# Kernel optimization log

Measured on AMD Instinct MI355X. Metric: run time of the kernel, lower is better.

Reference implementation:

```python
import jax, jax.numpy as jnp
import numpy as np

EPS = 0.1           # sinkhorn entropic regularizer (epsilon=0.1 in OT())
GAMMA = 1.0         # KL penalty on relaxed (row) marginal (gamma=1)
NUM_SK_ITERS = 3    # num_iters=3, final=False path
RHO_UPPER = 1.0
RHO_BASE = 0.1


def sigmoid_rampup(current, rampup_length):
    if rampup_length == 0:
        return 1.0
    current = np.clip(current, 0.0, rampup_length)
    phase = 1.0 - current / rampup_length
    return float(np.exp(-5.0 * phase * phase))


def set_rho(current, total):
    rho = sigmoid_rampup(current, total) * RHO_UPPER + RHO_BASE
    return min(rho, 1.0)


def setup_inputs() -> dict:
    key = jax.random.key(0)
    kx, ky = jax.random.split(key)
    x = jax.random.normal(kx, (8192, 1024), dtype=jnp.float32)
    y = jax.random.normal(ky, (2048, 1024), dtype=jnp.float32)
    return {"x": x, "y": y, "iterations": 100, "iterations_per_epoch": 20}


def _normalize_feature(x):
    # x = x - x.min(-1)[0].unsqueeze(-1)
    return x - jnp.min(x, axis=-1, keepdims=True)


def _cdist(x, y):
    # torch.cdist with p=2 (Euclidean)
    x2 = jnp.sum(x * x, axis=-1, keepdims=True)          # (N,1)
    y2 = jnp.sum(y * y, axis=-1)                         # (M,)
    d2 = x2 + y2[None, :] - 2.0 * (x @ y.T)              # (N,M)
    return jnp.sqrt(jnp.maximum(d2, 0.0))


def _semi_sinkhorn_stable(cost, rho):
    """Log-domain (stable) semi-relaxed Sinkhorn-Knopp.
    Column marginal is enforced exactly with total mass rho (curriculum mass);
    row marginal is relaxed via KL penalty gamma -> damped f update.
    Returns transport plan with sum(flow) == rho."""
    N, M = cost.shape
    lam = GAMMA / (GAMMA + EPS)
    loga = -np.log(N)                   # uniform row prior (prior=None)
    logb = np.log(rho) - np.log(M)      # uniform column marginal, mass rho
    logK = -cost / EPS                  # (N,M)
    f = jnp.zeros((N,), cost.dtype)
    g = jnp.zeros((M,), cost.dtype)
    lse = jax.scipy.special.logsumexp
    for _ in range(NUM_SK_ITERS):
        f = -lam * EPS * lse(logK + g[None, :] / EPS + logb, axis=1)
        g = -EPS * lse(logK + f[:, None] / EPS + loga, axis=0)
    flow = jnp.exp(logK + f[:, None] / EPS + g[None, :] / EPS + loga + logb)
    return flow


def reference(x, y, iterations, iterations_per_epoch):
    x = _normalize_feature(x)
    y = _normalize_feature(y)
    rho = set_rho(iterations, 10 * iterations_per_epoch)  # sigmoid rho schedule
    cost = _cdist(x, y)
    cost = cost / jnp.max(cost)
    flow = _semi_sinkhorn_stable(cost, rho)
    flow = flow / rho                                      # renormalize to total mass 1
    dist = jnp.sum(cost * flow)
    return flow, dist
```

## Files before the change

### kernel.cpp

```cpp
#include <hip/hip_runtime.h>
#include <math.h>

#define N_ROWS 8192
#define M_COLS 2048
#define K_DIM  1024
#define NM     ((size_t)N_ROWS * M_COLS)

#define LAM       0.9090909090909091f
#define LOG_M     7.624618986159398f

#define SKB 512
#define RPB (N_ROWS / SKB)

typedef __bf16 bf16x8 __attribute__((ext_vector_type(8)));
typedef float  f32x4  __attribute__((ext_vector_type(4)));
typedef unsigned short u16x8 __attribute__((ext_vector_type(8)));
typedef _Float16 h8 __attribute__((ext_vector_type(8)));


static __device__ __forceinline__ size_t xb_off(int i) {
    return ((size_t)(i >> 1) << 13) + 4096 + ((size_t)(i & 1) << 11);
}
static __device__ __forceinline__ size_t yb_off(int j) {
    return ((size_t)1 << 25) + ((size_t)(j >> 1) << 13) + 4096 + ((size_t)(j & 1) << 11);
}

__global__ void k_init(const int* __restrict__ iters, const int* __restrict__ ipe,
                       float* __restrict__ params, float* __restrict__ sigma,
                       unsigned int* __restrict__ d2max, float* __restrict__ dist)
{
    const int t = blockIdx.x * 256 + threadIdx.x;
    if (t < M_COLS) {
        sigma[t] = 0.0f;
        sigma[M_COLS + t] = 0.0f;
        sigma[2 * M_COLS + t] = 0.0f;
    }
    if (t == 0) {
        float ramp = 10.0f * (float)ipe[0];
        float rho;
        if (ramp == 0.0f) {
            rho = 1.1f;
        } else {
            float cur = fminf(fmaxf((float)iters[0], 0.0f), ramp);
            float phase = 1.0f - cur / ramp;
            rho = expf(-5.0f * phase * phase) + 0.1f;
        }
        rho = fminf(rho, 1.0f);
        params[0] = rho;
        params[1] = logf(rho) - LOG_M;
        *d2max = 0u;
        *dist = 0.0f;
    }
}

static __device__ __forceinline__ unsigned pk_bf16(float a, float b) {
#if __has_builtin(__builtin_amdgcn_cvt_pk_bf16_f32)
    typedef __bf16 bf16x2 __attribute__((ext_vector_type(2)));
    bf16x2 r = __builtin_amdgcn_cvt_pk_bf16_f32(a, b);
    return __builtin_bit_cast(unsigned, r);
#else
    unsigned ua = __float_as_uint(a), ub = __float_as_uint(b);
    ua += 0x7FFFu + ((ua >> 16) & 1u);
    ub += 0x7FFFu + ((ub >> 16) & 1u);
    return (ua >> 16) | (ub & 0xFFFF0000u);
#endif
}

static __device__ __forceinline__ bf16x8 lds_frag(const unsigned short* p) {
    return __builtin_bit_cast(bf16x8, *(const u16x8*)p);
}

static __device__ __forceinline__ void gload16(const void* g, void* l) {
    __builtin_amdgcn_global_load_lds(
        (const __attribute__((address_space(1))) unsigned int*)g,
        (__attribute__((address_space(3))) unsigned int*)l, 16, 0, 0);
}

__global__ __launch_bounds__(256) void rowstats_cvt(
    const float* __restrict__ X, const float* __restrict__ Y,
    unsigned char* __restrict__ outb,
    float* __restrict__ mx, float* __restrict__ sx, float* __restrict__ x2,
    float* __restrict__ my, float* __restrict__ sy, float* __restrict__ y2)
{
    const int b = blockIdx.x, tid = threadIdx.x;
    const bool isX = b < N_ROWS;
    const int row = isX ? b : b - N_ROWS;
    const float* src = isX ? (X + (size_t)row * K_DIM) : (Y + (size_t)row * K_DIM);
    const float4 v = ((const float4*)src)[tid];

    uint2 p; p.x = pk_bf16(v.x, v.y); p.y = pk_bf16(v.z, v.w);
    size_t off = isX ? xb_off(row) : yb_off(row);
    *(uint2*)(outb + off + (size_t)tid * 8) = p;

    float lmin = fminf(fminf(v.x, v.y), fminf(v.z, v.w));
    float lsum = v.x + v.y + v.z + v.w;
    float lsq  = v.x*v.x + v.y*v.y + v.z*v.z + v.w*v.w;

    __shared__ float rmin[256], rsum[256], rsq[256];
    rmin[tid] = lmin; rsum[tid] = lsum; rsq[tid] = lsq;
    __syncthreads();
    for (int s = 128; s > 0; s >>= 1) {
        if (tid < s) {
            rmin[tid] = fminf(rmin[tid], rmin[tid + s]);
            rsum[tid] += rsum[tid + s];
            rsq[tid]  += rsq[tid + s];
        }
        __syncthreads();
    }
    if (tid == 0) {
        float m = rmin[0], s = rsum[0], q = rsq[0];
        if (isX) { mx[row] = m; sx[row] = s; x2[row] = q - 2.f*m*s + (float)K_DIM*m*m; }
        else     { my[row] = m; sy[row] = s; y2[row] = q - 2.f*m*s + (float)K_DIM*m*m; }
    }
}

__global__ __launch_bounds__(256, 4) void gemm_cost_mfma(
    float* __restrict__ gbuf,
    const float* __restrict__ mx, const float* __restrict__ sx, const float* __restrict__ x2,
    const float* __restrict__ my, const float* __restrict__ sy, const float* __restrict__ y2,
    unsigned int* __restrict__ d2max)
{
    __shared__ unsigned short Ash[2][128 * 32];
    __shared__ unsigned short Bsh[2][128 * 32];
    __shared__ float rmax[256];

    const unsigned char* outb = (const unsigned char*)gbuf;
    const int tid   = threadIdx.x;
    const int lane  = tid & 63;
    const int wave  = tid >> 6;
    const int wi    = wave >> 1;
    const int wj    = wave & 1;
    const int row16 = lane & 15;
    const int quad  = lane >> 4;

    const int bid0 = blockIdx.y * 16 + blockIdx.x;
    const int bid  = (bid0 & 7) * 128 + (bid0 >> 3);
    const int i0 = (bid >> 4) * 128, j0 = (bid & 15) * 128;

    const int chA = (lane & 3) * 16;
    const unsigned char* pa[2];
    const unsigned char* pb[2];
    unsigned short* laA[2];
    unsigned short* lbB[2];
    #pragma unroll
    for (int p = 0; p < 2; ++p) {
        const int rt = (p * 4 + wave) * 16 + (lane >> 2);
        pa[p] = outb + xb_off(i0 + rt) + chA;
        pb[p] = outb + yb_off(j0 + rt) + chA;
        laA[p] = &Ash[0][(p * 4 + wave) * 512];
        lbB[p] = &Bsh[0][(p * 4 + wave) * 512];
    }

    f32x4 acc[4][4];
    #pragma unroll
    for (int u = 0; u < 4; ++u)
        #pragma unroll
        for (int v = 0; v < 4; ++v) acc[u][v] = (f32x4){0.f, 0.f, 0.f, 0.f};

#define STAGE(nb) do {                                        \
        gload16(pa[0], laA[0] + (nb) * 4096);                 \
        gload16(pa[1], laA[1] + (nb) * 4096);                 \
        gload16(pb[0], lbB[0] + (nb) * 4096);                 \
        gload16(pb[1], lbB[1] + (nb) * 4096);                 \
        pa[0] += 64; pa[1] += 64; pb[0] += 64; pb[1] += 64;   \
    } while (0)

#define COMPUTE(cb) do {                                                         \
        bf16x8 af[4], bfr[4];                                                    \
        _Pragma("unroll")                                                        \
        for (int t = 0; t < 4; ++t) {                                            \
            af[t]  = lds_frag(&Ash[cb][(wi * 64 + t * 16 + row16) * 32 + quad * 8]); \
            bfr[t] = lds_frag(&Bsh[cb][(wj * 64 + t * 16 + row16) * 32 + quad * 8]); \
        }                                                                        \
        _Pragma("unroll")                                                        \
        for (int ti = 0; ti < 4; ++ti)                                           \
            _Pragma("unroll")                                                    \
            for (int tj = 0; tj < 4; ++tj)                                       \
                acc[ti][tj] = __builtin_amdgcn_mfma_f32_16x16x32_bf16(           \
                    af[ti], bfr[tj], acc[ti][tj], 0, 0, 0);                      \
    } while (0)

    STAGE(0);
    __syncthreads();

#pragma unroll 1
    for (int it = 0; it < 15; ++it) {
        STAGE(1); COMPUTE(0); __syncthreads();
        STAGE(0); COMPUTE(1); __syncthreads();
    }
    STAGE(1); COMPUTE(0); __syncthreads();
    COMPUTE(1);

#undef STAGE
#undef COMPUTE

    _Float16* costh = (_Float16*)gbuf;
    float lmax = 0.0f;
    float myj[4], syj[4], yy[4];
    #pragma unroll
    for (int tj = 0; tj < 4; ++tj) {
        const int j = j0 + wj * 64 + tj * 16 + row16;
        myj[tj] = my[j]; syj[tj] = sy[j]; yy[tj] = y2[j];
    }
    #pragma unroll
    for (int ti = 0; ti < 4; ++ti) {
        #pragma unroll
        for (int reg = 0; reg < 4; ++reg) {
            const int i = i0 + wi * 64 + ti * 16 + quad * 4 + reg;
            const float mxi = mx[i], sxi = sx[i], xxi = x2[i];
            #pragma unroll
            for (int tj = 0; tj < 4; ++tj) {
                const int j = j0 + wj * 64 + tj * 16 + row16;
                float corr = mxi * syj[tj] + myj[tj] * sxi - (float)K_DIM * mxi * myj[tj];
                float d2 = xxi + yy[tj] - 2.0f * acc[ti][tj][reg] + 2.0f * corr;
                d2 = fmaxf(d2, 0.0f);
                lmax = fmaxf(lmax, d2);
                costh[(size_t)i * 4096 + j] = (_Float16)sqrtf(d2);
            }
        }
    }
    rmax[tid] = lmax;
    __syncthreads();
    for (int s = 128; s > 0; s >>= 1) {
        if (tid < s) rmax[tid] = fmaxf(rmax[tid], rmax[tid + s]);
        __syncthreads();
    }
    if (tid == 0) atomicMax(d2max, __float_as_uint(rmax[0]));
}

template<bool FIRST>
__global__ __launch_bounds__(256) void sk_iter(
    float* __restrict__ outbuf, const float* __restrict__ sigma,
    float* __restrict__ w, _Float16* __restrict__ gpart,
    const float* __restrict__ params, const unsigned int* __restrict__ d2max)
{
    const int tid  = threadIdx.x;
    const int lane = tid & 63;
    const int wave = tid >> 6;
    const int r0   = blockIdx.x * RPB;
    const float logb = params[1];

    _Float16* Eb = (_Float16*)outbuf;
    h8 E[RPB];

    #pragma unroll
    for (int r = 0; r < RPB; ++r)
        E[r] = __builtin_bit_cast(h8, *(const uint4*)(Eb + (size_t)(r0 + r) * 4096 + 8 * tid));

    if (FIRST) {
        const float invC10 = 10.0f * rsqrtf(__uint_as_float(*d2max));
        #pragma unroll
        for (int r = 0; r < RPB; ++r) {
            h8 e;
            #pragma unroll
            for (int c = 0; c < 8; ++c)
                e[c] = (_Float16)__expf(-(float)E[r][c] * invC10);
            E[r] = e;
            *(uint4*)(Eb + (size_t)(r0 + r) * 4096 + 8 * tid) = __builtin_bit_cast(uint4, e);
        }
    }

    float u8[8];
    if (FIRST) {
        #pragma unroll
        for (int c = 0; c < 8; ++c) u8[c] = 1.0f;
    } else {
        float4 sa = *(const float4*)(sigma + 8 * tid);
        float4 sb = *(const float4*)(sigma + 8 * tid + 4);
        u8[0] = (float)N_ROWS / sa.x; u8[1] = (float)N_ROWS / sa.y;
        u8[2] = (float)N_ROWS / sa.z; u8[3] = (float)N_ROWS / sa.w;
        u8[4] = (float)N_ROWS / sb.x; u8[5] = (float)N_ROWS / sb.y;
        u8[6] = (float)N_ROWS / sb.z; u8[7] = (float)N_ROWS / sb.w;
    }

    float pr[RPB];
    #pragma unroll
    for (int r = 0; r < RPB; ++r) {
        float s = 0.0f;
        #pragma unroll
        for (int c = 0; c < 8; ++c) s += (float)E[r][c] * u8[c];
        pr[r] = s;
    }
    #pragma unroll
    for (int r = 0; r < RPB; ++r)
        #pragma unroll
        for (int off = 32; off > 0; off >>= 1)
            pr[r] += __shfl_xor(pr[r], off, 64);

    __shared__ float R[RPB][4];
    __shared__ float W[RPB];
    if (lane == 0)
        #pragma unroll
        for (int r = 0; r < RPB; ++r) R[r][wave] = pr[r];
    __syncthreads();
    if (tid < RPB) {
        float t = R[tid][0] + R[tid][1] + R[tid][2] + R[tid][3];
        float wr = __expf(-LAM * (logb + __logf(t)));
        W[tid] = wr;
        w[r0 + tid] = wr;
    }
    __syncthreads();

    float p[8] = {0.f, 0.f, 0.f, 0.f, 0.f, 0.f, 0.f, 0.f};
    #pragma unroll
    for (int r = 0; r < RPB; ++r) {
        const float wr = W[r];
        #pragma unroll
        for (int c = 0; c < 8; ++c) p[c] += (float)E[r][c] * wr;
    }
    h8 ph;
    #pragma unroll
    for (int c = 0; c < 8; ++c) ph[c] = (_Float16)p[c];
    *(uint4*)(gpart + (size_t)blockIdx.x * M_COLS + 8 * tid) = __builtin_bit_cast(uint4, ph);
}

__global__ __launch_bounds__(256) void sk_gred(
    const _Float16* __restrict__ gpart, float* __restrict__ sigma)
{
    const int col = (blockIdx.x & 7) * 256 + threadIdx.x;
    const int b0  = (blockIdx.x >> 3) * (SKB / 8);
    float s = 0.0f;
    #pragma unroll 8
    for (int b = 0; b < SKB / 8; ++b)
        s += (float)gpart[(size_t)(b0 + b) * M_COLS + col];
    atomicAdd(&sigma[col], s);
}

__global__ __launch_bounds__(256) void flow_dist(
    float* __restrict__ outbuf, const float* __restrict__ w,
    const float* __restrict__ sigma, float* __restrict__ dist)
{
    const int tid = threadIdx.x;
    const int r0  = blockIdx.x * RPB;
    const float invNM = 1.0f / ((float)N_ROWS * (float)M_COLS);
    _Float16* Eb = (_Float16*)outbuf;

    h8 E[RPB];
    #pragma unroll
    for (int r = 0; r < RPB; ++r)
        E[r] = __builtin_bit_cast(h8, *(const uint4*)(Eb + (size_t)(r0 + r) * 4096 + 8 * tid));

    __shared__ float W[RPB];
    if (tid < RPB) W[tid] = w[r0 + tid];

    float4 sA = *(const float4*)(sigma + 8 * tid);
    float4 sB = *(const float4*)(sigma + 8 * tid + 4);
    float u8[8];
    u8[0] = (float)N_ROWS / sA.x; u8[1] = (float)N_ROWS / sA.y;
    u8[2] = (float)N_ROWS / sA.z; u8[3] = (float)N_ROWS / sA.w;
    u8[4] = (float)N_ROWS / sB.x; u8[5] = (float)N_ROWS / sB.y;
    u8[6] = (float)N_ROWS / sB.z; u8[7] = (float)N_ROWS / sB.w;

    __syncthreads();

    float local = 0.0f;
    #pragma unroll
    for (int r = 0; r < RPB; ++r) {
        const float wr = W[r];
        float fl[8];
        #pragma unroll
        for (int c = 0; c < 8; ++c) {
            float e = (float)E[r][c];
            float o = e * wr * u8[c] * invNM;
            fl[c] = o;
            float cn = -0.1f * __logf(fmaxf(e, 1e-7f));
            local += cn * o;
        }
        float4 o0 = {fl[0], fl[1], fl[2], fl[3]};
        float4 o1 = {fl[4], fl[5], fl[6], fl[7]};
        float* frow = outbuf + (size_t)(r0 + r) * M_COLS + 8 * tid;
        *(float4*)frow = o0;
        *(float4*)(frow + 4) = o1;
    }

    __shared__ float red[256];
    red[tid] = local;
    __syncthreads();
    for (int s = 128; s > 0; s >>= 1) {
        if (tid < s) red[tid] += red[tid + s];
        __syncthreads();
    }
    if (tid == 0) atomicAdd(dist, red[0]);
}

extern "C" void kernel_launch(void* const* d_in, const int* in_sizes, int n_in,
                              void* d_out, int out_size, void* d_ws, size_t ws_size,
                              hipStream_t stream)
{
    const float* x     = (const float*)d_in[0];
    const float* y     = (const float*)d_in[1];
    const int*   iters = (const int*)d_in[2];
    const int*   ipe   = (const int*)d_in[3];
    float* out = (float*)d_out;
    float* ws  = (float*)d_ws;

    float*        params = ws;
    unsigned int* d2max  = (unsigned int*)(ws + 8);
    float* w     = ws + 16;
    float* sigma = w + N_ROWS;
    float* mx = sigma + 3 * M_COLS;
    float* sx = mx + N_ROWS;
    float* x2 = sx + N_ROWS;
    float* my = x2 + N_ROWS;
    float* sy = my + M_COLS;
    float* y2 = sy + M_COLS;
    _Float16* gpart = (_Float16*)(y2 + M_COLS);

    float* sigma0 = sigma;
    float* sigma1 = sigma + M_COLS;
    float* sigma2 = sigma + 2 * M_COLS;

    float* dist = out + NM;

    k_init<<<8, 256, 0, stream>>>(iters, ipe, params, sigma, d2max, dist);
    rowstats_cvt<<<N_ROWS + M_COLS, 256, 0, stream>>>(
        x, y, (unsigned char*)out, mx, sx, x2, my, sy, y2);
    gemm_cost_mfma<<<dim3(M_COLS / 128, N_ROWS / 128), 256, 0, stream>>>(
        out, mx, sx, x2, my, sy, y2, d2max);

    sk_iter<true><<<SKB, 256, 0, stream>>>(out, nullptr, w, gpart, params, d2max);
    sk_gred<<<64, 256, 0, stream>>>(gpart, sigma0);
    sk_iter<false><<<SKB, 256, 0, stream>>>(out, sigma0, w, gpart, params, d2max);
    sk_gred<<<64, 256, 0, stream>>>(gpart, sigma1);
    sk_iter<false><<<SKB, 256, 0, stream>>>(out, sigma1, w, gpart, params, d2max);
    sk_gred<<<64, 256, 0, stream>>>(gpart, sigma2);

    flow_dist<<<SKB, 256, 0, stream>>>(out, w, sigma2, dist);
}
```

Measured before the change: 213.2 us.

## Fuse init into rowstats, recompute exp from cost, replace gred with atomics

Folds the init kernel into the first block of rowstats_cvt and drops the separate column-reduction kernels, so each Sinkhorn pass atomically adds its column partial sums straight into sigma. The fp16 cost is kept in place and the kernel exp(-C/eps) is recomputed in every pass instead of being written back once. flow_dist computes the normalized cost directly rather than through log of the kernel entries. This removes four kernel launches and the gpart round trip, at the cost of extra exp work per pass and heavy float atomic contention: 512 blocks add into 2048 addresses each pass.

```diff
diff --git a/kernel.cpp b/kernel.cpp
--- a/kernel.cpp
+++ b/kernel.cpp
@@ -23,34 +23,6 @@
 }
 static __device__ __forceinline__ size_t yb_off(int j) {
     return ((size_t)1 << 25) + ((size_t)(j >> 1) << 13) + 4096 + ((size_t)(j & 1) << 11);
-}
-
-__global__ void k_init(const int* __restrict__ iters, const int* __restrict__ ipe,
-                       float* __restrict__ params, float* __restrict__ sigma,
-                       unsigned int* __restrict__ d2max, float* __restrict__ dist)
-{
-    const int t = blockIdx.x * 256 + threadIdx.x;
-    if (t < M_COLS) {
-        sigma[t] = 0.0f;
-        sigma[M_COLS + t] = 0.0f;
-        sigma[2 * M_COLS + t] = 0.0f;
-    }
-    if (t == 0) {
-        float ramp = 10.0f * (float)ipe[0];
-        float rho;
-        if (ramp == 0.0f) {
-            rho = 1.1f;
-        } else {
-            float cur = fminf(fmaxf((float)iters[0], 0.0f), ramp);
-            float phase = 1.0f - cur / ramp;
-            rho = expf(-5.0f * phase * phase) + 0.1f;
-        }
-        rho = fminf(rho, 1.0f);
-        params[0] = rho;
-        params[1] = logf(rho) - LOG_M;
-        *d2max = 0u;
-        *dist = 0.0f;
-    }
 }
 
 static __device__ __forceinline__ unsigned pk_bf16(float a, float b) {
@@ -79,10 +51,35 @@
 __global__ __launch_bounds__(256) void rowstats_cvt(
     const float* __restrict__ X, const float* __restrict__ Y,
     unsigned char* __restrict__ outb,
+    const int* __restrict__ iters, const int* __restrict__ ipe,
+    float* __restrict__ params, float* __restrict__ sigma,
+    unsigned int* __restrict__ d2max, float* __restrict__ dist,
     float* __restrict__ mx, float* __restrict__ sx, float* __restrict__ x2,
     float* __restrict__ my, float* __restrict__ sy, float* __restrict__ y2)
 {
     const int b = blockIdx.x, tid = threadIdx.x;
+
+    if (b == 0) {
+        #pragma unroll 1
+        for (int i = tid; i < 3 * M_COLS; i += 256) sigma[i] = 0.0f;
+        if (tid == 0) {
+            float ramp = 10.0f * (float)ipe[0];
+            float rho;
+            if (ramp == 0.0f) {
+                rho = 1.1f;
+            } else {
+                float cur = fminf(fmaxf((float)iters[0], 0.0f), ramp);
+                float phase = 1.0f - cur / ramp;
+                rho = expf(-5.0f * phase * phase) + 0.1f;
+            }
+            rho = fminf(rho, 1.0f);
+            params[0] = rho;
+            params[1] = logf(rho) - LOG_M;
+            *d2max = 0u;
+            *dist = 0.0f;
+        }
+    }
+
     const bool isX = b < N_ROWS;
     const int row = isX ? b : b - N_ROWS;
     const float* src = isX ? (X + (size_t)row * K_DIM) : (Y + (size_t)row * K_DIM);
@@ -228,10 +225,10 @@
     if (tid == 0) atomicMax(d2max, __float_as_uint(rmax[0]));
 }
 
-template<bool FIRST>
-__global__ __launch_bounds__(256) void sk_iter(
-    float* __restrict__ outbuf, const float* __restrict__ sigma,
-    float* __restrict__ w, _Float16* __restrict__ gpart,
+template<int IT>
+__global__ __launch_bounds__(256) void sk_pass(
+    const float* __restrict__ outbuf, float* __restrict__ sigma,
+    float* __restrict__ w,
     const float* __restrict__ params, const unsigned int* __restrict__ d2max)
 {
     const int tid  = threadIdx.x;
@@ -239,34 +236,28 @@
     const int wave = tid >> 6;
     const int r0   = blockIdx.x * RPB;
     const float logb = params[1];
-
-    _Float16* Eb = (_Float16*)outbuf;
+    const float invC10 = 10.0f * rsqrtf(__uint_as_float(*d2max));
+
+    const _Float16* Eb = (const _Float16*)outbuf;
     h8 E[RPB];
-
-    #pragma unroll
-    for (int r = 0; r < RPB; ++r)
-        E[r] = __builtin_bit_cast(h8, *(const uint4*)(Eb + (size_t)(r0 + r) * 4096 + 8 * tid));
-
-    if (FIRST) {
-        const float invC10 = 10.0f * rsqrtf(__uint_as_float(*d2max));
-        #pragma unroll
-        for (int r = 0; r < RPB; ++r) {
-            h8 e;
-            #pragma unroll
-            for (int c = 0; c < 8; ++c)
-                e[c] = (_Float16)__expf(-(float)E[r][c] * invC10);
-            E[r] = e;
-            *(uint4*)(Eb + (size_t)(r0 + r) * 4096 + 8 * tid) = __builtin_bit_cast(uint4, e);
-        }
+    #pragma unroll
+    for (int r = 0; r < RPB; ++r) {
+        h8 c = __builtin_bit_cast(h8, *(const uint4*)(Eb + (size_t)(r0 + r) * 4096 + 8 * tid));
+        h8 e;
+        #pragma unroll
+        for (int k = 0; k < 8; ++k)
+            e[k] = (_Float16)__expf(-(float)c[k] * invC10);
+        E[r] = e;
     }
 
     float u8[8];
-    if (FIRST) {
+    if constexpr (IT == 0) {
         #pragma unroll
         for (int c = 0; c < 8; ++c) u8[c] = 1.0f;
     } else {
-        float4 sa = *(const float4*)(sigma + 8 * tid);
-        float4 sb = *(const float4*)(sigma + 8 * tid + 4);
+        const float* sg = sigma + (IT - 1) * M_COLS;
+        const float4 sa = *(const float4*)(sg + 8 * tid);
+        const float4 sb = *(const float4*)(sg + 8 * tid + 4);
         u8[0] = (float)N_ROWS / sa.x; u8[1] = (float)N_ROWS / sa.y;
         u8[2] = (float)N_ROWS / sa.z; u8[3] = (float)N_ROWS / sa.w;
         u8[4] = (float)N_ROWS / sb.x; u8[5] = (float)N_ROWS / sb.y;
@@ -297,7 +288,7 @@
         float t = R[tid][0] + R[tid][1] + R[tid][2] + R[tid][3];
         float wr = __expf(-LAM * (logb + __logf(t)));
         W[tid] = wr;
-        w[r0 + tid] = wr;
+        if constexpr (IT == 2) w[r0 + tid] = wr;
     }
     __syncthreads();
 
@@ -308,43 +299,33 @@
         #pragma unroll
         for (int c = 0; c < 8; ++c) p[c] += (float)E[r][c] * wr;
     }
-    h8 ph;
-    #pragma unroll
-    for (int c = 0; c < 8; ++c) ph[c] = (_Float16)p[c];
-    *(uint4*)(gpart + (size_t)blockIdx.x * M_COLS + 8 * tid) = __builtin_bit_cast(uint4, ph);
-}
-
-__global__ __launch_bounds__(256) void sk_gred(
-    const _Float16* __restrict__ gpart, float* __restrict__ sigma)
-{
-    const int col = (blockIdx.x & 7) * 256 + threadIdx.x;
-    const int b0  = (blockIdx.x >> 3) * (SKB / 8);
-    float s = 0.0f;
-    #pragma unroll 8
-    for (int b = 0; b < SKB / 8; ++b)
-        s += (float)gpart[(size_t)(b0 + b) * M_COLS + col];
-    atomicAdd(&sigma[col], s);
+    float* sg1 = sigma + IT * M_COLS;
+    #pragma unroll
+    for (int c = 0; c < 8; ++c) atomicAdd(&sg1[8 * tid + c], p[c]);
 }
 
 __global__ __launch_bounds__(256) void flow_dist(
     float* __restrict__ outbuf, const float* __restrict__ w,
-    const float* __restrict__ sigma, float* __restrict__ dist)
+    const float* __restrict__ sigma2, const unsigned int* __restrict__ d2max,
+    float* __restrict__ dist)
 {
     const int tid = threadIdx.x;
     const int r0  = blockIdx.x * RPB;
     const float invNM = 1.0f / ((float)N_ROWS * (float)M_COLS);
-    _Float16* Eb = (_Float16*)outbuf;
-
-    h8 E[RPB];
+    const float invC10 = 10.0f * rsqrtf(__uint_as_float(*d2max));
+    const float inv01  = 0.1f * invC10;
+    const _Float16* Eb = (const _Float16*)outbuf;
+
+    h8 C[RPB];
     #pragma unroll
     for (int r = 0; r < RPB; ++r)
-        E[r] = __builtin_bit_cast(h8, *(const uint4*)(Eb + (size_t)(r0 + r) * 4096 + 8 * tid));
+        C[r] = __builtin_bit_cast(h8, *(const uint4*)(Eb + (size_t)(r0 + r) * 4096 + 8 * tid));
 
     __shared__ float W[RPB];
     if (tid < RPB) W[tid] = w[r0 + tid];
 
-    float4 sA = *(const float4*)(sigma + 8 * tid);
-    float4 sB = *(const float4*)(sigma + 8 * tid + 4);
+    const float4 sA = *(const float4*)(sigma2 + 8 * tid);
+    const float4 sB = *(const float4*)(sigma2 + 8 * tid + 4);
     float u8[8];
     u8[0] = (float)N_ROWS / sA.x; u8[1] = (float)N_ROWS / sA.y;
     u8[2] = (float)N_ROWS / sA.z; u8[3] = (float)N_ROWS / sA.w;
@@ -360,11 +341,11 @@
         float fl[8];
         #pragma unroll
         for (int c = 0; c < 8; ++c) {
-            float e = (float)E[r][c];
+            float cst = (float)C[r][c];
+            float e = __expf(-cst * invC10);
             float o = e * wr * u8[c] * invNM;
             fl[c] = o;
-            float cn = -0.1f * __logf(fmaxf(e, 1e-7f));
-            local += cn * o;
+            local += (cst * inv01) * o;
         }
         float4 o0 = {fl[0], fl[1], fl[2], fl[3]};
         float4 o1 = {fl[4], fl[5], fl[6], fl[7]};
@@ -404,26 +385,18 @@
     float* my = x2 + N_ROWS;
     float* sy = my + M_COLS;
     float* y2 = sy + M_COLS;
-    _Float16* gpart = (_Float16*)(y2 + M_COLS);
-
-    float* sigma0 = sigma;
-    float* sigma1 = sigma + M_COLS;
-    float* sigma2 = sigma + 2 * M_COLS;
 
     float* dist = out + NM;
 
-    k_init<<<8, 256, 0, stream>>>(iters, ipe, params, sigma, d2max, dist);
     rowstats_cvt<<<N_ROWS + M_COLS, 256, 0, stream>>>(
-        x, y, (unsigned char*)out, mx, sx, x2, my, sy, y2);
+        x, y, (unsigned char*)out, iters, ipe, params, sigma, d2max, dist,
+        mx, sx, x2, my, sy, y2);
     gemm_cost_mfma<<<dim3(M_COLS / 128, N_ROWS / 128), 256, 0, stream>>>(
         out, mx, sx, x2, my, sy, y2, d2max);
 
-    sk_iter<true><<<SKB, 256, 0, stream>>>(out, nullptr, w, gpart, params, d2max);
-    sk_gred<<<64, 256, 0, stream>>>(gpart, sigma0);
-    sk_iter<false><<<SKB, 256, 0, stream>>>(out, sigma0, w, gpart, params, d2max);
-    sk_gred<<<64, 256, 0, stream>>>(gpart, sigma1);
-    sk_iter<false><<<SKB, 256, 0, stream>>>(out, sigma1, w, gpart, params, d2max);
-    sk_gred<<<64, 256, 0, stream>>>(gpart, sigma2);
-
-    flow_dist<<<SKB, 256, 0, stream>>>(out, w, sigma2, dist);
-}
+    sk_pass<0><<<SKB, 256, 0, stream>>>(out, sigma, w, params, d2max);
+    sk_pass<1><<<SKB, 256, 0, stream>>>(out, sigma, w, params, d2max);
+    sk_pass<2><<<SKB, 256, 0, stream>>>(out, sigma, w, params, d2max);
+
+    flow_dist<<<SKB, 256, 0, stream>>>(out, w, sigma + 2 * M_COLS, d2max, dist);
+}
```

After: 525.3 us. 146% more time.
